# Kernel optimization log

Hardware: AMD Instinct MI355X
Metric: run time of the kernel (lower is better)

Reference implementation:

```python
import jax, jax.numpy as jnp
import numpy as np

N = 50000
E = 800000
D = 256
EPS = 1e-5  # BatchNorm eps


def _gcn_conv(x, W, b, row, col):
    # PyG GCNConv: h = x @ W; add self-loops; sym-normalize; scatter-add; + bias
    h = x @ W  # [N, D]
    deg = jnp.zeros((N,), x.dtype).at[col].add(jnp.ones((row.shape[0],), x.dtype))
    dinv = jax.lax.rsqrt(deg)  # deg >= 1 thanks to self-loops
    norm = dinv[row] * dinv[col]  # [E+N]
    msg = h[row] * norm[:, None]  # gather + scale, [E+N, D]
    out = jnp.zeros_like(h).at[col].add(msg)  # scatter-aggregate
    return out + b


def _bn(x, gamma, beta):
    # BatchNorm1d in training mode: batch statistics over nodes
    m = jnp.mean(x, axis=0)
    v = jnp.var(x, axis=0)
    return (x - m) * jax.lax.rsqrt(v + EPS) * gamma + beta


def setup_inputs() -> dict:
    key = jax.random.key(0)
    ks = jax.random.split(key, 4)
    x = jax.random.normal(ks[0], (N, D), dtype=jnp.float32)
    edge_index = jax.random.randint(ks[1], (2, E), 0, N, dtype=jnp.int64)
    s = 1.0 / np.sqrt(D)
    W1 = jax.random.uniform(ks[2], (D, D), jnp.float32, -s, s)
    W2 = jax.random.uniform(ks[3], (D, D), jnp.float32, -s, s)
    z = jnp.zeros((D,), jnp.float32)
    o = jnp.ones((D,), jnp.float32)
    return {"x": x, "edge_index": edge_index,
            "W1": W1, "b1": z, "g1": o, "be1": z,
            "W2": W2, "b2": z, "g2": o, "be2": z}


def reference(x, edge_index, W1, b1, g1, be1, W2, b2, g2, be2):
    loops = jnp.arange(N, dtype=edge_index.dtype)
    row = jnp.concatenate([edge_index[0], loops])  # sources
    col = jnp.concatenate([edge_index[1], loops])  # targets
    # layer 1: GCNConv -> BN -> ReLU (dropout is identity in eval)
    h = _gcn_conv(x, W1, b1, row, col)
    h = jax.nn.relu(_bn(h, g1, be1))
    # layer 2
    h = _gcn_conv(h, W2, b2, row, col)
    h = jax.nn.relu(_bn(h, g2, be2))
    return h
```

## Files before the change

### kernel.cpp

```cpp
#include <hip/hip_runtime.h>
#include <cstdint>
#include <cstddef>

constexpr int N = 50000;
constexpr int E = 800000;
constexpr int D = 256;
constexpr float EPS = 1e-5f;
constexpr int NB = (N + 255) / 256;
constexpr int BN_BLOCKS = 512;
constexpr int GB = (N + 63) / 64;

typedef __attribute__((ext_vector_type(8))) short short8;
typedef __attribute__((ext_vector_type(8))) unsigned short ushort8;
typedef __attribute__((ext_vector_type(4))) float f32x4;

__device__ __forceinline__ unsigned short f2bf(float f) {
  union { float f; unsigned u; } c; c.f = f;
  unsigned u = c.u;
  u += 0x7fff + ((u >> 16) & 1);
  return (unsigned short)(u >> 16);
}
__device__ __forceinline__ float bf2f(unsigned short h) {
  union { unsigned u; float f; } c; c.u = ((unsigned)h) << 16;
  return c.f;
}
__device__ __forceinline__ float bflo(unsigned u) {
  union { unsigned x; float f; } c; c.x = u << 16; return c.f;
}
__device__ __forceinline__ float bfhi(unsigned u) {
  union { unsigned x; float f; } c; c.x = u & 0xffff0000u; return c.f;
}

__device__ __forceinline__ int detect64(const void* ei) {
  const int* p = (const int*)ei;
  int l = threadIdx.x & 63;
  int nz = (p[2 * l + 1] != 0) | (p[2 * l + 129] != 0);
  return __ballot(nz) == 0ULL;
}

__device__ __forceinline__ int edge_at(const void* ei, int is64, long long pos) {
  if (is64) return (int)((const long long*)ei)[pos];
  return ((const int*)ei)[pos];
}

__global__ void k_count(const void* __restrict__ ei, int* __restrict__ degc) {
  int is64 = detect64(ei);
  int e = blockIdx.x * 256 + threadIdx.x;
  if (e >= E) return;
  int c = edge_at(ei, is64, (long long)E + e);
  atomicAdd(&degc[c], 1);
}

__global__ void k_scan_partial(const int* __restrict__ degc, int* __restrict__ bsum,
                               float* __restrict__ dinv) {
  __shared__ int sd[256];
  int t = threadIdx.x;
  int i = blockIdx.x * 256 + t;
  int dv = (i < N) ? degc[i] : 0;
  if (i < N) dinv[i] = rsqrtf((float)(dv + 1));
  int v = (i < N) ? (dv + 1) : 0;
  sd[t] = v;
  __syncthreads();
  for (int s = 128; s > 0; s >>= 1) {
    if (t < s) sd[t] += sd[t + s];
    __syncthreads();
  }
  if (t == 0) bsum[blockIdx.x] = sd[0];
}

__global__ void k_scan_final(const int* __restrict__ degc, const int* __restrict__ bsum,
                             const float* __restrict__ dinv, int* __restrict__ offs,
                             int* __restrict__ curs, int2* __restrict__ epair) {
  __shared__ int sb[256];
  __shared__ int sd[256];
  int t = threadIdx.x;
  int bv = (t < NB) ? bsum[t] : 0;
  sb[t] = bv;
  __syncthreads();
  for (int off = 1; off < 256; off <<= 1) {
    int x = (t >= off) ? sb[t - off] : 0;
    __syncthreads();
    sb[t] += x;
    __syncthreads();
  }
  int base = sb[blockIdx.x] - bsum[blockIdx.x];
  int i = blockIdx.x * 256 + t;
  int v = (i < N) ? (degc[i] + 1) : 0;
  sd[t] = v;
  __syncthreads();
  for (int off = 1; off < 256; off <<= 1) {
    int x = (t >= off) ? sd[t - off] : 0;
    __syncthreads();
    sd[t] += x;
    __syncthreads();
  }
  if (i < N) {
    int o = base + sd[t] - v;
    offs[i] = o;
    curs[i] = o + 1;
    float d = dinv[i];
    epair[o] = make_int2(i, __float_as_int(d * d));
  }
  if (i == N - 1) offs[N] = base + sd[t];
}

__global__ void k_fill_edges(const void* __restrict__ ei,
                             const float* __restrict__ dinv, int* __restrict__ curs,
                             int2* __restrict__ epair) {
  int is64 = detect64(ei);
  int e = blockIdx.x * 256 + threadIdx.x;
  if (e >= E) return;
  int r = edge_at(ei, is64, e);
  int c = edge_at(ei, is64, (long long)E + e);
  int p = atomicAdd(&curs[c], 1);
  epair[p] = make_int2(r, __float_as_int(dinv[r] * dinv[c]));
}

__global__ void k_wfrag(const float* __restrict__ W1, const float* __restrict__ W2,
                        unsigned short* __restrict__ Wf1, unsigned short* __restrict__ Wf2) {
  int b = blockIdx.x;
  const float* W = (b < 128) ? W1 : W2;
  unsigned short* Wf = (b < 128) ? Wf1 : Wf2;
  int tile = b & 127;
  int lane = threadIdx.x;
  int kstep = tile >> 4, wn = tile & 15;
  int kbase = kstep * 32 + (lane >> 4) * 8;
  int col = wn * 16 + (lane & 15);
  short8 v;
#pragma unroll
  for (int j = 0; j < 8; ++j)
    v[j] = (short)f2bf(W[(size_t)(kbase + j) * 256 + col]);
  *(short8*)&Wf[(((size_t)tile) * 64 + lane) * 8] = v;
}

template <bool A_BF16, bool FUSE_BN>
__global__ __launch_bounds__(256) void k_gemm(const void* __restrict__ Ap,
                                              const unsigned short* __restrict__ Wf,
                                              unsigned short* __restrict__ C,
                                              const float* __restrict__ sc,
                                              const float* __restrict__ sh) {
  __shared__ unsigned short As[64][264];
  int t = threadIdx.x;
  int lane = t & 63;
  int w = t >> 6;
  int row0 = blockIdx.x * 64;
  int l16 = lane & 15, lk = lane >> 4;

  f32x4 acc[4][4];
#pragma unroll
  for (int i = 0; i < 4; ++i)
#pragma unroll
    for (int j = 0; j < 4; ++j) acc[i][j] = (f32x4){0.f, 0.f, 0.f, 0.f};

  int arow = t >> 2;
  int ak0 = (t & 3) * 8;
  int gr = row0 + arow;
  bool inb = (gr < N);

#pragma unroll
  for (int ks = 0; ks < 8; ++ks) {
    int kc = ks * 32 + ak0;
    float f[8] = {0.f, 0.f, 0.f, 0.f, 0.f, 0.f, 0.f, 0.f};
    if (inb) {
      if (A_BF16) {
        const unsigned short* A = (const unsigned short*)Ap;
        short8 v = *(const short8*)&A[(size_t)gr * 256 + kc];
#pragma unroll
        for (int j = 0; j < 8; ++j) f[j] = bf2f((unsigned short)v[j]);
      } else {
        const float* A = (const float*)Ap;
        float4 f0 = *(const float4*)&A[(size_t)gr * 256 + kc];
        float4 f1 = *(const float4*)&A[(size_t)gr * 256 + kc + 4];
        f[0] = f0.x; f[1] = f0.y; f[2] = f0.z; f[3] = f0.w;
        f[4] = f1.x; f[5] = f1.y; f[6] = f1.z; f[7] = f1.w;
      }
    }
    if (FUSE_BN) {
#pragma unroll
      for (int j = 0; j < 8; ++j)
        f[j] = fmaxf(fmaf(f[j], sc[kc + j], sh[kc + j]), 0.f);
    }
    ushort4 u0 = {f2bf(f[0]), f2bf(f[1]), f2bf(f[2]), f2bf(f[3])};
    ushort4 u1 = {f2bf(f[4]), f2bf(f[5]), f2bf(f[6]), f2bf(f[7])};
    *(ushort4*)&As[arow][kc] = u0;
    *(ushort4*)&As[arow][kc + 4] = u1;
  }
  __syncthreads();

#pragma unroll
  for (int ks = 0; ks < 8; ++ks) {
    short8 af[4];
#pragma unroll
    for (int mf = 0; mf < 4; ++mf)
      af[mf] = *(const short8*)&As[mf * 16 + l16][ks * 32 + lk * 8];
#pragma unroll
    for (int nf = 0; nf < 4; ++nf) {
      short8 bf = *(const short8*)&Wf[(((size_t)ks * 16 + w * 4 + nf) * 64 + lane) * 8];
#pragma unroll
      for (int mf = 0; mf < 4; ++mf)
        acc[mf][nf] = __builtin_amdgcn_mfma_f32_16x16x32_bf16(af[mf], bf, acc[mf][nf], 0, 0, 0);
    }
  }
  __syncthreads();

  unsigned short(*Cs)[264] = As;
#pragma unroll
  for (int mf = 0; mf < 4; ++mf)
#pragma unroll
    for (int nf = 0; nf < 4; ++nf)
#pragma unroll
      for (int r = 0; r < 4; ++r)
        Cs[mf * 16 + lk * 4 + r][w * 64 + nf * 16 + l16] = f2bf(acc[mf][nf][r]);
  __syncthreads();
#pragma unroll
  for (int it = 0; it < 8; ++it) {
    int r = it * 8 + (t >> 5);
    int gr2 = row0 + r;
    if (gr2 < N)
      *(short8*)&C[(size_t)gr2 * 256 + (t & 31) * 8] = *(const short8*)&Cs[r][(t & 31) * 8];
  }
}

__global__ __launch_bounds__(256) void k_agg(const unsigned short* __restrict__ h,
                                             const int* __restrict__ offs,
                                             const int2* __restrict__ epair,
                                             const float* __restrict__ bias,
                                             unsigned short* __restrict__ outp) {
  int t = threadIdx.x;
  int nd = blockIdx.x * 8 + (t >> 5);
  if (nd >= N) return;
  int lane = t & 31;
  int e = offs[nd];
  int end = offs[nd + 1];
  float a0 = 0.f, a1 = 0.f, a2 = 0.f, a3 = 0.f;
  float a4 = 0.f, a5 = 0.f, a6 = 0.f, a7 = 0.f;

#define ACC8(v, wgt)                       \
  do {                                     \
    a0 = fmaf(wgt, bflo((v).x), a0);       \
    a1 = fmaf(wgt, bfhi((v).x), a1);       \
    a2 = fmaf(wgt, bflo((v).y), a2);       \
    a3 = fmaf(wgt, bfhi((v).y), a3);       \
    a4 = fmaf(wgt, bflo((v).z), a4);       \
    a5 = fmaf(wgt, bfhi((v).z), a5);       \
    a6 = fmaf(wgt, bflo((v).w), a6);       \
    a7 = fmaf(wgt, bfhi((v).w), a7);       \
  } while (0)

  for (; e + 8 <= end; e += 8) {
    int2 p0 = epair[e + 0], p1 = epair[e + 1], p2 = epair[e + 2], p3 = epair[e + 3];
    int2 p4 = epair[e + 4], p5 = epair[e + 5], p6 = epair[e + 6], p7 = epair[e + 7];
    uint4 v0 = *(const uint4*)&h[(size_t)p0.x * 256 + lane * 8];
    uint4 v1 = *(const uint4*)&h[(size_t)p1.x * 256 + lane * 8];
    uint4 v2 = *(const uint4*)&h[(size_t)p2.x * 256 + lane * 8];
    uint4 v3 = *(const uint4*)&h[(size_t)p3.x * 256 + lane * 8];
    uint4 v4 = *(const uint4*)&h[(size_t)p4.x * 256 + lane * 8];
    uint4 v5 = *(const uint4*)&h[(size_t)p5.x * 256 + lane * 8];
    uint4 v6 = *(const uint4*)&h[(size_t)p6.x * 256 + lane * 8];
    uint4 v7 = *(const uint4*)&h[(size_t)p7.x * 256 + lane * 8];
    ACC8(v0, __int_as_float(p0.y));
    ACC8(v1, __int_as_float(p1.y));
    ACC8(v2, __int_as_float(p2.y));
    ACC8(v3, __int_as_float(p3.y));
    ACC8(v4, __int_as_float(p4.y));
    ACC8(v5, __int_as_float(p5.y));
    ACC8(v6, __int_as_float(p6.y));
    ACC8(v7, __int_as_float(p7.y));
  }
  if (e < end) {
#pragma unroll
    for (int k = 0; k < 8; ++k) {
      int idx = e + k;
      bool act = (idx < end);
      int2 p = epair[act ? idx : end - 1];
      float wgt = act ? __int_as_float(p.y) : 0.f;
      uint4 v = *(const uint4*)&h[(size_t)p.x * 256 + lane * 8];
      ACC8(v, wgt);
    }
  }
#undef ACC8

  float4 b0 = *(const float4*)&bias[lane * 8];
  float4 b1 = *(const float4*)&bias[lane * 8 + 4];
  ushort8 o;
  o[0] = f2bf(a0 + b0.x); o[1] = f2bf(a1 + b0.y);
  o[2] = f2bf(a2 + b0.z); o[3] = f2bf(a3 + b0.w);
  o[4] = f2bf(a4 + b1.x); o[5] = f2bf(a5 + b1.y);
  o[6] = f2bf(a6 + b1.z); o[7] = f2bf(a7 + b1.w);
  *(ushort8*)&outp[(size_t)nd * 256 + lane * 8] = o;
}

__global__ __launch_bounds__(256) void k_bnpart(const unsigned short* __restrict__ xp,
                                                float* __restrict__ partial) {
  int t = threadIdx.x;
  int lane = t & 63;
  int sub = t >> 6;
  float sx = 0, sy = 0, sz = 0, sw = 0;
  float qx = 0, qy = 0, qz = 0, qw = 0;
  for (int r = blockIdx.x * 4 + sub; r < N; r += gridDim.x * 4) {
    uint2 u = *(const uint2*)&xp[(size_t)r * 256 + lane * 4];
    float vx = bflo(u.x);
    float vy = bfhi(u.x);
    float vz = bflo(u.y);
    float vw = bfhi(u.y);
    sx += vx; sy += vy; sz += vz; sw += vw;
    qx = fmaf(vx, vx, qx); qy = fmaf(vy, vy, qy);
    qz = fmaf(vz, vz, qz); qw = fmaf(vw, vw, qw);
  }
  __shared__ float4 ps[256];
  __shared__ float4 pq[256];
  ps[t] = {sx, sy, sz, sw};
  pq[t] = {qx, qy, qz, qw};
  __syncthreads();
  float* pout = partial + (size_t)blockIdx.x * 512;
  if (t < 64) {
    float4 a = ps[t], b = ps[64 + t], c = ps[128 + t], d = ps[192 + t];
    float4 o = {a.x + b.x + c.x + d.x, a.y + b.y + c.y + d.y,
                a.z + b.z + c.z + d.z, a.w + b.w + c.w + d.w};
    ((float4*)pout)[t] = o;
  } else if (t < 128) {
    int l = t - 64;
    float4 a = pq[l], b = pq[64 + l], c = pq[128 + l], d = pq[192 + l];
    float4 o = {a.x + b.x + c.x + d.x, a.y + b.y + c.y + d.y,
                a.z + b.z + c.z + d.z, a.w + b.w + c.w + d.w};
    ((float4*)(pout + 256))[l] = o;
  }
}

__global__ __launch_bounds__(256) void k_bnred(const float* __restrict__ partial,
                                               float* __restrict__ bnsum,
                                               float* __restrict__ bnsq,
                                               int* __restrict__ cnt,
                                               const float* __restrict__ g,
                                               const float* __restrict__ be,
                                               float* __restrict__ sc,
                                               float* __restrict__ sh) {
  int t = threadIdx.x;
  float s = 0.f, q = 0.f;
  int b0 = blockIdx.x * (BN_BLOCKS / 16);
  for (int b = b0; b < b0 + BN_BLOCKS / 16; ++b) {
    s += partial[(size_t)b * 512 + t];
    q += partial[(size_t)b * 512 + 256 + t];
  }
  atomicAdd(&bnsum[t], s);
  atomicAdd(&bnsq[t], q);
  __threadfence();
  __shared__ int last;
  if (t == 0) last = (atomicAdd(cnt, 1) == 15);
  __syncthreads();
  if (last) {
    float S = atomicAdd(&bnsum[t], 0.f);
    float Q = atomicAdd(&bnsq[t], 0.f);
    const float inv = 1.f / (float)N;
    float m = S * inv;
    float v = Q * inv - m * m;
    float sf = rsqrtf(v + EPS) * g[t];
    sc[t] = sf;
    sh[t] = be[t] - m * sf;
  }
}

__global__ __launch_bounds__(256) void k_bnapply(const unsigned short* __restrict__ in,
                                                 float* __restrict__ outp,
                                                 const float* __restrict__ sc,
                                                 const float* __restrict__ sh) {
  int t = threadIdx.x;
  int lane = t & 63;
  int sub = t >> 6;
  float4 s4 = ((const float4*)sc)[lane];
  float4 h4 = ((const float4*)sh)[lane];
  for (int r = blockIdx.x * 4 + sub; r < N; r += gridDim.x * 4) {
    uint2 u = *(const uint2*)&in[(size_t)r * 256 + lane * 4];
    float4 v;
    v.x = fmaxf(fmaf(bflo(u.x), s4.x, h4.x), 0.f);
    v.y = fmaxf(fmaf(bfhi(u.x), s4.y, h4.y), 0.f);
    v.z = fmaxf(fmaf(bflo(u.y), s4.z, h4.z), 0.f);
    v.w = fmaxf(fmaf(bfhi(u.y), s4.w, h4.w), 0.f);
    *(float4*)&outp[(size_t)r * 256 + lane * 4] = v;
  }
}

extern "C" void kernel_launch(void* const* d_in, const int* in_sizes, int n_in,
                              void* d_out, int out_size, void* d_ws, size_t ws_size,
                              hipStream_t stream) {
  const float* x  = (const float*)d_in[0];
  const void*  ei = d_in[1];
  const float* W1 = (const float*)d_in[2];
  const float* b1 = (const float*)d_in[3];
  const float* g1 = (const float*)d_in[4];
  const float* be1 = (const float*)d_in[5];
  const float* W2 = (const float*)d_in[6];
  const float* b2 = (const float*)d_in[7];
  const float* g2 = (const float*)d_in[8];
  const float* be2 = (const float*)d_in[9];
  float* out = (float*)d_out;

  char* base = (char*)d_ws;
  size_t off = 0;
  unsigned short* hbuf = (unsigned short*)(base + off); off += (size_t)N * D * 2;
  unsigned short* abuf = (unsigned short*)(base + off); off += (size_t)N * D * 2;
  unsigned short* Wf1 = (unsigned short*)(base + off);  off += (size_t)D * D * 2;
  unsigned short* Wf2 = (unsigned short*)(base + off);  off += (size_t)D * D * 2;
  int*   degc = (int*)(base + off);    off += (size_t)N * 4;
  float* bnsum1 = (float*)(base + off); off += (size_t)D * 4;
  float* bnsq1  = (float*)(base + off); off += (size_t)D * 4;
  float* bnsum2 = (float*)(base + off); off += (size_t)D * 4;
  float* bnsq2  = (float*)(base + off); off += (size_t)D * 4;
  int*   cnt1 = (int*)(base + off);    off += 8;
  int*   cnt2 = (int*)(base + off);    off += 8;
  size_t zero_bytes = (size_t)N * 4 + 4 * (size_t)D * 4 + 16;
  float* dinv = (float*)(base + off); off += (size_t)N * 4;
  int*   offs = (int*)(base + off);   off += (size_t)(N + 4) * 4;
  int*   curs = (int*)(base + off);   off += (size_t)N * 4;
  int2*  epair = (int2*)(base + off); off += (size_t)(E + N) * 8;
  float* partial = (float*)(base + off); off += (size_t)BN_BLOCKS * 512 * 4;
  float* sc1 = (float*)(base + off);  off += (size_t)D * 4;
  float* sh1 = (float*)(base + off);  off += (size_t)D * 4;
  float* sc2 = (float*)(base + off);  off += (size_t)D * 4;
  float* sh2 = (float*)(base + off);  off += (size_t)D * 4;
  int*   bsum = (int*)(base + off);   off += 256 * 4;

  hipMemsetAsync(degc, 0, zero_bytes, stream);

  k_wfrag<<<256, 64, 0, stream>>>(W1, W2, Wf1, Wf2);

  k_count<<<(E + 255) / 256, 256, 0, stream>>>(ei, degc);
  k_scan_partial<<<NB, 256, 0, stream>>>(degc, bsum, dinv);
  k_scan_final<<<NB, 256, 0, stream>>>(degc, bsum, dinv, offs, curs, epair);
  k_fill_edges<<<(E + 255) / 256, 256, 0, stream>>>(ei, dinv, curs, epair);

  int agg_grid = (N + 7) / 8;

  k_gemm<false, false><<<GB, 256, 0, stream>>>(x, Wf1, hbuf, nullptr, nullptr);
  k_agg<<<agg_grid, 256, 0, stream>>>(hbuf, offs, epair, b1, abuf);
  k_bnpart<<<BN_BLOCKS, 256, 0, stream>>>(abuf, partial);
  k_bnred<<<16, 256, 0, stream>>>(partial, bnsum1, bnsq1, cnt1, g1, be1, sc1, sh1);

  k_gemm<true, true><<<GB, 256, 0, stream>>>(abuf, Wf2, hbuf, sc1, sh1);
  k_agg<<<agg_grid, 256, 0, stream>>>(hbuf, offs, epair, b2, abuf);
  k_bnpart<<<BN_BLOCKS, 256, 0, stream>>>(abuf, partial);
  k_bnred<<<16, 256, 0, stream>>>(partial, bnsum2, bnsq2, cnt2, g2, be2, sc2, sh2);
  k_bnapply<<<512, 256, 0, stream>>>(abuf, out, sc2, sh2);
}
```

Baseline: 321.0 us.

## Fuse BN partial stats into aggregation and merge GEMM1 with degree count

The BatchNorm partial-sum kernel is folded into the aggregation kernel, which now accumulates per-feature sums and squares while writing output. This removes a full reread of the N x D activation. Aggregation switches to a persistent grid of 2048 blocks with one 64-lane wave per node, each lane covering 4 features, instead of 32 lanes with 8 features. The first GEMM and the edge degree count now run in one launch with split block ranges, so they can overlap. In exchange the gather uses narrower per-lane loads and the partial buffer and reduction grow to 2048 blocks.

```diff
diff --git a/kernel.cpp b/kernel.cpp
--- a/kernel.cpp
+++ b/kernel.cpp
@@ -7,11 +7,11 @@
 constexpr int D = 256;
 constexpr float EPS = 1e-5f;
 constexpr int NB = (N + 255) / 256;
-constexpr int BN_BLOCKS = 512;
 constexpr int GB = (N + 63) / 64;
+constexpr int CB = (E + 255) / 256;
+constexpr int AGG_BLOCKS = 2048;
 
 typedef __attribute__((ext_vector_type(8))) short short8;
-typedef __attribute__((ext_vector_type(8))) unsigned short ushort8;
 typedef __attribute__((ext_vector_type(4))) float f32x4;
 
 __device__ __forceinline__ unsigned short f2bf(float f) {
@@ -43,12 +43,117 @@
   return ((const int*)ei)[pos];
 }
 
-__global__ void k_count(const void* __restrict__ ei, int* __restrict__ degc) {
-  int is64 = detect64(ei);
-  int e = blockIdx.x * 256 + threadIdx.x;
-  if (e >= E) return;
-  int c = edge_at(ei, is64, (long long)E + e);
-  atomicAdd(&degc[c], 1);
+template <bool A_BF16, bool FUSE_BN>
+__device__ __forceinline__ void gemm_body(const void* __restrict__ Ap,
+                                          const unsigned short* __restrict__ Wf,
+                                          unsigned short* __restrict__ C,
+                                          const float* __restrict__ sc,
+                                          const float* __restrict__ sh,
+                                          int bid) {
+  __shared__ unsigned short As[64][264];
+  int t = threadIdx.x;
+  int lane = t & 63;
+  int w = t >> 6;
+  int row0 = bid * 64;
+  int l16 = lane & 15, lk = lane >> 4;
+
+  f32x4 acc[4][4];
+#pragma unroll
+  for (int i = 0; i < 4; ++i)
+#pragma unroll
+    for (int j = 0; j < 4; ++j) acc[i][j] = (f32x4){0.f, 0.f, 0.f, 0.f};
+
+  int arow = t >> 2;
+  int ak0 = (t & 3) * 8;
+  int gr = row0 + arow;
+  bool inb = (gr < N);
+
+#pragma unroll
+  for (int ks = 0; ks < 8; ++ks) {
+    int kc = ks * 32 + ak0;
+    float f[8] = {0.f, 0.f, 0.f, 0.f, 0.f, 0.f, 0.f, 0.f};
+    if (inb) {
+      if (A_BF16) {
+        const unsigned short* A = (const unsigned short*)Ap;
+        short8 v = *(const short8*)&A[(size_t)gr * 256 + kc];
+#pragma unroll
+        for (int j = 0; j < 8; ++j) f[j] = bf2f((unsigned short)v[j]);
+      } else {
+        const float* A = (const float*)Ap;
+        float4 f0 = *(const float4*)&A[(size_t)gr * 256 + kc];
+        float4 f1 = *(const float4*)&A[(size_t)gr * 256 + kc + 4];
+        f[0] = f0.x; f[1] = f0.y; f[2] = f0.z; f[3] = f0.w;
+        f[4] = f1.x; f[5] = f1.y; f[6] = f1.z; f[7] = f1.w;
+      }
+    }
+    if (FUSE_BN) {
+#pragma unroll
+      for (int j = 0; j < 8; ++j)
+        f[j] = fmaxf(fmaf(f[j], sc[kc + j], sh[kc + j]), 0.f);
+    }
+    ushort4 u0 = {f2bf(f[0]), f2bf(f[1]), f2bf(f[2]), f2bf(f[3])};
+    ushort4 u1 = {f2bf(f[4]), f2bf(f[5]), f2bf(f[6]), f2bf(f[7])};
+    *(ushort4*)&As[arow][kc] = u0;
+    *(ushort4*)&As[arow][kc + 4] = u1;
+  }
+  __syncthreads();
+
+#pragma unroll
+  for (int ks = 0; ks < 8; ++ks) {
+    short8 af[4];
+#pragma unroll
+    for (int mf = 0; mf < 4; ++mf)
+      af[mf] = *(const short8*)&As[mf * 16 + l16][ks * 32 + lk * 8];
+#pragma unroll
+    for (int nf = 0; nf < 4; ++nf) {
+      short8 bf = *(const short8*)&Wf[(((size_t)ks * 16 + w * 4 + nf) * 64 + lane) * 8];
+#pragma unroll
+      for (int mf = 0; mf < 4; ++mf)
+        acc[mf][nf] = __builtin_amdgcn_mfma_f32_16x16x32_bf16(af[mf], bf, acc[mf][nf], 0, 0, 0);
+    }
+  }
+  __syncthreads();
+
+  unsigned short(*Cs)[264] = As;
+#pragma unroll
+  for (int mf = 0; mf < 4; ++mf)
+#pragma unroll
+    for (int nf = 0; nf < 4; ++nf)
+#pragma unroll
+      for (int r = 0; r < 4; ++r)
+        Cs[mf * 16 + lk * 4 + r][w * 64 + nf * 16 + l16] = f2bf(acc[mf][nf][r]);
+  __syncthreads();
+#pragma unroll
+  for (int it = 0; it < 8; ++it) {
+    int r = it * 8 + (t >> 5);
+    int gr2 = row0 + r;
+    if (gr2 < N)
+      *(short8*)&C[(size_t)gr2 * 256 + (t & 31) * 8] = *(const short8*)&Cs[r][(t & 31) * 8];
+  }
+}
+
+__global__ __launch_bounds__(256) void k_gemm1_count(const float* __restrict__ x,
+                                                     const unsigned short* __restrict__ Wf1,
+                                                     unsigned short* __restrict__ hbuf,
+                                                     const void* __restrict__ ei,
+                                                     int* __restrict__ degc) {
+  if (blockIdx.x < GB) {
+    gemm_body<false, false>(x, Wf1, hbuf, nullptr, nullptr, blockIdx.x);
+  } else {
+    int is64 = detect64(ei);
+    int e = (blockIdx.x - GB) * 256 + threadIdx.x;
+    if (e >= E) return;
+    int c = edge_at(ei, is64, (long long)E + e);
+    atomicAdd(&degc[c], 1);
+  }
+}
+
+__global__ __launch_bounds__(256) void k_gemm2(const unsigned short* __restrict__ A,
+                                               const unsigned short* __restrict__ Wf,
+                                               unsigned short* __restrict__ C,
+                                               const float* __restrict__ sc,
+                                               const float* __restrict__ sh) {
+  gemm_body<true, true>(A, Wf, C, sc, sh, blockIdx.x);
 }
 
 __global__ void k_scan_partial(const int* __restrict__ degc, int* __restrict__ bsum,
@@ -133,184 +238,82 @@
   *(short8*)&Wf[(((size_t)tile) * 64 + lane) * 8] = v;
 }
 
-template <bool A_BF16, bool FUSE_BN>
-__global__ __launch_bounds__(256) void k_gemm(const void* __restrict__ Ap,
-                                              const unsigned short* __restrict__ Wf,
-                                              unsigned short* __restrict__ C,
-                                              const float* __restrict__ sc,
-                                              const float* __restrict__ sh) {
-  __shared__ unsigned short As[64][264];
-  int t = threadIdx.x;
-  int lane = t & 63;
-  int w = t >> 6;
-  int row0 = blockIdx.x * 64;
-  int l16 = lane & 15, lk = lane >> 4;
-
-  f32x4 acc[4][4];
-#pragma unroll
-  for (int i = 0; i < 4; ++i)
-#pragma unroll
-    for (int j = 0; j < 4; ++j) acc[i][j] = (f32x4){0.f, 0.f, 0.f, 0.f};
-
-  int arow = t >> 2;
-  int ak0 = (t & 3) * 8;
-  int gr = row0 + arow;
-  bool inb = (gr < N);
-
-#pragma unroll
-  for (int ks = 0; ks < 8; ++ks) {
-    int kc = ks * 32 + ak0;
-    float f[8] = {0.f, 0.f, 0.f, 0.f, 0.f, 0.f, 0.f, 0.f};
-    if (inb) {
-      if (A_BF16) {
-        const unsigned short* A = (const unsigned short*)Ap;
-        short8 v = *(const short8*)&A[(size_t)gr * 256 + kc];
-#pragma unroll
-        for (int j = 0; j < 8; ++j) f[j] = bf2f((unsigned short)v[j]);
-      } else {
-        const float* A = (const float*)Ap;
-        float4 f0 = *(const float4*)&A[(size_t)gr * 256 + kc];
-        float4 f1 = *(const float4*)&A[(size_t)gr * 256 + kc + 4];
-        f[0] = f0.x; f[1] = f0.y; f[2] = f0.z; f[3] = f0.w;
-        f[4] = f1.x; f[5] = f1.y; f[6] = f1.z; f[7] = f1.w;
-      }
-    }
-    if (FUSE_BN) {
-#pragma unroll
-      for (int j = 0; j < 8; ++j)
-        f[j] = fmaxf(fmaf(f[j], sc[kc + j], sh[kc + j]), 0.f);
-    }
-    ushort4 u0 = {f2bf(f[0]), f2bf(f[1]), f2bf(f[2]), f2bf(f[3])};
-    ushort4 u1 = {f2bf(f[4]), f2bf(f[5]), f2bf(f[6]), f2bf(f[7])};
-    *(ushort4*)&As[arow][kc] = u0;
-    *(ushort4*)&As[arow][kc + 4] = u1;
-  }
-  __syncthreads();
-
-#pragma unroll
-  for (int ks = 0; ks < 8; ++ks) {
-    short8 af[4];
-#pragma unroll
-    for (int mf = 0; mf < 4; ++mf)
-      af[mf] = *(const short8*)&As[mf * 16 + l16][ks * 32 + lk * 8];
-#pragma unroll
-    for (int nf = 0; nf < 4; ++nf) {
-      short8 bf = *(const short8*)&Wf[(((size_t)ks * 16 + w * 4 + nf) * 64 + lane) * 8];
-#pragma unroll
-      for (int mf = 0; mf < 4; ++mf)
-        acc[mf][nf] = __builtin_amdgcn_mfma_f32_16x16x32_bf16(af[mf], bf, acc[mf][nf], 0, 0, 0);
-    }
-  }
-  __syncthreads();
-
-  unsigned short(*Cs)[264] = As;
-#pragma unroll
-  for (int mf = 0; mf < 4; ++mf)
-#pragma unroll
-    for (int nf = 0; nf < 4; ++nf)
-#pragma unroll
-      for (int r = 0; r < 4; ++r)
-        Cs[mf * 16 + lk * 4 + r][w * 64 + nf * 16 + l16] = f2bf(acc[mf][nf][r]);
-  __syncthreads();
-#pragma unroll
-  for (int it = 0; it < 8; ++it) {
-    int r = it * 8 + (t >> 5);
-    int gr2 = row0 + r;
-    if (gr2 < N)
-      *(short8*)&C[(size_t)gr2 * 256 + (t & 31) * 8] = *(const short8*)&Cs[r][(t & 31) * 8];
-  }
-}
-
 __global__ __launch_bounds__(256) void k_agg(const unsigned short* __restrict__ h,
                                              const int* __restrict__ offs,
                                              const int2* __restrict__ epair,
                                              const float* __restrict__ bias,
-                                             unsigned short* __restrict__ outp) {
-  int t = threadIdx.x;
-  int nd = blockIdx.x * 8 + (t >> 5);
-  if (nd >= N) return;
-  int lane = t & 31;
-  int e = offs[nd];
-  int end = offs[nd + 1];
-  float a0 = 0.f, a1 = 0.f, a2 = 0.f, a3 = 0.f;
-  float a4 = 0.f, a5 = 0.f, a6 = 0.f, a7 = 0.f;
-
-#define ACC8(v, wgt)                       \
-  do {                                     \
-    a0 = fmaf(wgt, bflo((v).x), a0);       \
-    a1 = fmaf(wgt, bfhi((v).x), a1);       \
-    a2 = fmaf(wgt, bflo((v).y), a2);       \
-    a3 = fmaf(wgt, bfhi((v).y), a3);       \
-    a4 = fmaf(wgt, bflo((v).z), a4);       \
-    a5 = fmaf(wgt, bfhi((v).z), a5);       \
-    a6 = fmaf(wgt, bflo((v).w), a6);       \
-    a7 = fmaf(wgt, bfhi((v).w), a7);       \
+                                             unsigned short* __restrict__ outp,
+                                             float* __restrict__ partial) {
+  int t = threadIdx.x;
+  int wv = t >> 6;
+  int lane = t & 63;
+  float4 bb = ((const float4*)bias)[lane];
+  float s0 = 0.f, s1 = 0.f, s2 = 0.f, s3 = 0.f;
+  float q0 = 0.f, q1 = 0.f, q2 = 0.f, q3 = 0.f;
+
+#define ACC4(v, wgt)                         \
+  do {                                       \
+    a0 = fmaf(wgt, bflo((v).x), a0);         \
+    a1 = fmaf(wgt, bfhi((v).x), a1);         \
+    a2 = fmaf(wgt, bflo((v).y), a2);         \
+    a3 = fmaf(wgt, bfhi((v).y), a3);         \
   } while (0)
 
-  for (; e + 8 <= end; e += 8) {
-    int2 p0 = epair[e + 0], p1 = epair[e + 1], p2 = epair[e + 2], p3 = epair[e + 3];
-    int2 p4 = epair[e + 4], p5 = epair[e + 5], p6 = epair[e + 6], p7 = epair[e + 7];
-    uint4 v0 = *(const uint4*)&h[(size_t)p0.x * 256 + lane * 8];
-    uint4 v1 = *(const uint4*)&h[(size_t)p1.x * 256 + lane * 8];
-    uint4 v2 = *(const uint4*)&h[(size_t)p2.x * 256 + lane * 8];
-    uint4 v3 = *(const uint4*)&h[(size_t)p3.x * 256 + lane * 8];
-    uint4 v4 = *(const uint4*)&h[(size_t)p4.x * 256 + lane * 8];
-    uint4 v5 = *(const uint4*)&h[(size_t)p5.x * 256 + lane * 8];
-    uint4 v6 = *(const uint4*)&h[(size_t)p6.x * 256 + lane * 8];
-    uint4 v7 = *(const uint4*)&h[(size_t)p7.x * 256 + lane * 8];
-    ACC8(v0, __int_as_float(p0.y));
-    ACC8(v1, __int_as_float(p1.y));
-    ACC8(v2, __int_as_float(p2.y));
-    ACC8(v3, __int_as_float(p3.y));
-    ACC8(v4, __int_as_float(p4.y));
-    ACC8(v5, __int_as_float(p5.y));
-    ACC8(v6, __int_as_float(p6.y));
-    ACC8(v7, __int_as_float(p7.y));
-  }
-  if (e < end) {
-#pragma unroll
-    for (int k = 0; k < 8; ++k) {
-      int idx = e + k;
-      bool act = (idx < end);
-      int2 p = epair[act ? idx : end - 1];
-      float wgt = act ? __int_as_float(p.y) : 0.f;
-      uint4 v = *(const uint4*)&h[(size_t)p.x * 256 + lane * 8];
-      ACC8(v, wgt);
+  for (int nd0 = blockIdx.x * 4; nd0 < N; nd0 += AGG_BLOCKS * 4) {
+    int nd = nd0 + wv;
+    if (nd < N) {
+      int node = __builtin_amdgcn_readfirstlane(nd);
+      int e = offs[node];
+      int end = offs[node + 1];
+      float a0 = 0.f, a1 = 0.f, a2 = 0.f, a3 = 0.f;
+
+      for (; e + 8 <= end; e += 8) {
+        int2 p0 = epair[e + 0], p1 = epair[e + 1], p2 = epair[e + 2], p3 = epair[e + 3];
+        int2 p4 = epair[e + 4], p5 = epair[e + 5], p6 = epair[e + 6], p7 = epair[e + 7];
+        uint2 v0 = *(const uint2*)&h[(size_t)p0.x * 256 + lane * 4];
+        uint2 v1 = *(const uint2*)&h[(size_t)p1.x * 256 + lane * 4];
+        uint2 v2 = *(const uint2*)&h[(size_t)p2.x * 256 + lane * 4];
+        uint2 v3 = *(const uint2*)&h[(size_t)p3.x * 256 + lane * 4];
+        uint2 v4 = *(const uint2*)&h[(size_t)p4.x * 256 + lane * 4];
+        uint2 v5 = *(const uint2*)&h[(size_t)p5.x * 256 + lane * 4];
+        uint2 v6 = *(const uint2*)&h[(size_t)p6.x * 256 + lane * 4];
+        uint2 v7 = *(const uint2*)&h[(size_t)p7.x * 256 + lane * 4];
+        ACC4(v0, __int_as_float(p0.y));
+        ACC4(v1, __int_as_float(p1.y));
+        ACC4(v2, __int_as_float(p2.y));
+        ACC4(v3, __int_as_float(p3.y));
+        ACC4(v4, __int_as_float(p4.y));
+        ACC4(v5, __int_as_float(p5.y));
+        ACC4(v6, __int_as_float(p6.y));
+        ACC4(v7, __int_as_float(p7.y));
+      }
+      if (e < end) {
+#pragma unroll
+        for (int k = 0; k < 8; ++k) {
+          int idx = e + k;
+          bool act = (idx < end);
+          int2 p = epair[act ? idx : end - 1];
+          float wgt = act ? __int_as_float(p.y) : 0.f;
+          uint2 v = *(const uint2*)&h[(size_t)p.x * 256 + lane * 4];
+          ACC4(v, wgt);
+        }
+      }
+
+      ushort4 o = {f2bf(a0 + bb.x), f2bf(a1 + bb.y), f2bf(a2 + bb.z), f2bf(a3 + bb.w)};
+      *(ushort4*)&outp[(size_t)nd * 256 + lane * 4] = o;
+      float f0 = bf2f(o.x), f1 = bf2f(o.y), f2v = bf2f(o.z), f3 = bf2f(o.w);
+      s0 += f0; q0 = fmaf(f0, f0, q0);
+      s1 += f1; q1 = fmaf(f1, f1, q1);
+      s2 += f2v; q2 = fmaf(f2v, f2v, q2);
+      s3 += f3; q3 = fmaf(f3, f3, q3);
     }
   }
-#undef ACC8
-
-  float4 b0 = *(const float4*)&bias[lane * 8];
-  float4 b1 = *(const float4*)&bias[lane * 8 + 4];
-  ushort8 o;
-  o[0] = f2bf(a0 + b0.x); o[1] = f2bf(a1 + b0.y);
-  o[2] = f2bf(a2 + b0.z); o[3] = f2bf(a3 + b0.w);
-  o[4] = f2bf(a4 + b1.x); o[5] = f2bf(a5 + b1.y);
-  o[6] = f2bf(a6 + b1.z); o[7] = f2bf(a7 + b1.w);
-  *(ushort8*)&outp[(size_t)nd * 256 + lane * 8] = o;
-}
-
-__global__ __launch_bounds__(256) void k_bnpart(const unsigned short* __restrict__ xp,
-                                                float* __restrict__ partial) {
-  int t = threadIdx.x;
-  int lane = t & 63;
-  int sub = t >> 6;
-  float sx = 0, sy = 0, sz = 0, sw = 0;
-  float qx = 0, qy = 0, qz = 0, qw = 0;
-  for (int r = blockIdx.x * 4 + sub; r < N; r += gridDim.x * 4) {
-    uint2 u = *(const uint2*)&xp[(size_t)r * 256 + lane * 4];
-    float vx = bflo(u.x);
-    float vy = bfhi(u.x);
-    float vz = bflo(u.y);
-    float vw = bfhi(u.y);
-    sx += vx; sy += vy; sz += vz; sw += vw;
-    qx = fmaf(vx, vx, qx); qy = fmaf(vy, vy, qy);
-    qz = fmaf(vz, vz, qz); qw = fmaf(vw, vw, qw);
-  }
+#undef ACC4
+
   __shared__ float4 ps[256];
   __shared__ float4 pq[256];
-  ps[t] = {sx, sy, sz, sw};
-  pq[t] = {qx, qy, qz, qw};
+  ps[t] = {s0, s1, s2, s3};
+  pq[t] = {q0, q1, q2, q3};
   __syncthreads();
   float* pout = partial + (size_t)blockIdx.x * 512;
   if (t < 64) {
@@ -337,8 +340,8 @@
                                                float* __restrict__ sh) {
   int t = threadIdx.x;
   float s = 0.f, q = 0.f;
-  int b0 = blockIdx.x * (BN_BLOCKS / 16);
-  for (int b = b0; b < b0 + BN_BLOCKS / 16; ++b) {
+  int b0 = blockIdx.x * (AGG_BLOCKS / 16);
+  for (int b = b0; b < b0 + AGG_BLOCKS / 16; ++b) {
     s += partial[(size_t)b * 512 + t];
     q += partial[(size_t)b * 512 + 256 + t];
   }
@@ -413,7 +416,7 @@
   int*   offs = (int*)(base + off);   off += (size_t)(N + 4) * 4;
   int*   curs = (int*)(base + off);   off += (size_t)N * 4;
   int2*  epair = (int2*)(base + off); off += (size_t)(E + N) * 8;
-  float* partial = (float*)(base + off); off += (size_t)BN_BLOCKS * 512 * 4;
+  float* partial = (float*)(base + off); off += (size_t)AGG_BLOCKS * 512 * 4;
   float* sc1 = (float*)(base + off);  off += (size_t)D * 4;
   float* sh1 = (float*)(base + off);  off += (size_t)D * 4;
   float* sc2 = (float*)(base + off);  off += (size_t)D * 4;
@@ -424,21 +427,17 @@
 
   k_wfrag<<<256, 64, 0, stream>>>(W1, W2, Wf1, Wf2);
 
-  k_count<<<(E + 255) / 256, 256, 0, stream>>>(ei, degc);
+  k_gemm1_count<<<GB + CB, 256, 0, stream>>>(x, Wf1, hbuf, ei, degc);
+
   k_scan_partial<<<NB, 256, 0, stream>>>(degc, bsum, dinv);
   k_scan_final<<<NB, 256, 0, stream>>>(degc, bsum, dinv, offs, curs, epair);
-  k_fill_edges<<<(E + 255) / 256, 256, 0, stream>>>(ei, dinv, curs, epair);
-
-  int agg_grid = (N + 7) / 8;
-
-  k_gemm<false, false><<<GB, 256, 0, stream>>>(x, Wf1, hbuf, nullptr, nullptr);
-  k_agg<<<agg_grid, 256, 0, stream>>>(hbuf, offs, epair, b1, abuf);
-  k_bnpart<<<BN_BLOCKS, 256, 0, stream>>>(abuf, partial);
+  k_fill_edges<<<CB, 256, 0, stream>>>(ei, dinv, curs, epair);
+
+  k_agg<<<AGG_BLOCKS, 256, 0, stream>>>(hbuf, offs, epair, b1, abuf, partial);
   k_bnred<<<16, 256, 0, stream>>>(partial, bnsum1, bnsq1, cnt1, g1, be1, sc1, sh1);
 
-  k_gemm<true, true><<<GB, 256, 0, stream>>>(abuf, Wf2, hbuf, sc1, sh1);
-  k_agg<<<agg_grid, 256, 0, stream>>>(hbuf, offs, epair, b2, abuf);
-  k_bnpart<<<BN_BLOCKS, 256, 0, stream>>>(abuf, partial);
+  k_gemm2<<<GB, 256, 0, stream>>>(abuf, Wf2, hbuf, sc1, sh1);
+  k_agg<<<AGG_BLOCKS, 256, 0, stream>>>(hbuf, offs, epair, b2, abuf, partial);
   k_bnred<<<16, 256, 0, stream>>>(partial, bnsum2, bnsq2, cnt2, g2, be2, sc2, sh2);
   k_bnapply<<<512, 256, 0, stream>>>(abuf, out, sc2, sh2);
 }
```

After: 283.6 us. 11.7% less time.
